# Kernel optimization log

Hardware: AMD Instinct MI355X
Metric: run time of the kernel (lower is better)

The kernel has to match this reference:

```python
import jax, jax.numpy as jnp
import numpy as np
import math

IMG, P, C, D, DEPTH, H, MLP, NCLS, B = 224, 16, 3, 768, 12, 12, 3072, 1000, 32
G = IMG // P          # 14 patches per side
N = G * G             # 196 patches
S = N + 1             # 197 tokens (cls + patches)
DK = D // H
PD = P * P * C        # 768 flattened patch dim


def layer_norm(x, g, b, eps=1e-5):
    mu = jnp.mean(x, axis=-1, keepdims=True)
    var = jnp.mean((x - mu) ** 2, axis=-1, keepdims=True)
    return (x - mu) * jax.lax.rsqrt(var + eps) * g + b


def setup_inputs() -> dict:
    key = jax.random.key(0)
    ks = iter(jax.random.split(key, 32))
    nrm = lambda shape, s=0.02: jax.random.normal(next(ks), shape, jnp.float32) * s
    inp = {
        'x': jax.random.normal(next(ks), (B, C, IMG, IMG), jnp.float32),
        'patch_W': nrm((PD, D)), 'patch_b': jnp.zeros((D,)),
        'cls_token': nrm((1, 1, D)), 'pos_embed': nrm((1, S, D)),
        'Wq': nrm((DEPTH, D, D)), 'bq': jnp.zeros((DEPTH, D)),
        'Wk': nrm((DEPTH, D, D)), 'bk': jnp.zeros((DEPTH, D)),
        'Wv': nrm((DEPTH, D, D)), 'bv': jnp.zeros((DEPTH, D)),
        'Wo': nrm((DEPTH, D, D)), 'bo': jnp.zeros((DEPTH, D)),
        'ln1_g': jnp.ones((DEPTH, D)), 'ln1_b': jnp.zeros((DEPTH, D)),
        'ln2_g': jnp.ones((DEPTH, D)), 'ln2_b': jnp.zeros((DEPTH, D)),
        'W1': nrm((DEPTH, D, MLP)), 'b1': jnp.zeros((DEPTH, MLP)),
        'W2': nrm((DEPTH, MLP, D)), 'b2': jnp.zeros((DEPTH, D)),
        'lnp_g': jnp.ones((D,)), 'lnp_b': jnp.zeros((D,)),
        'head_W': nrm((D, NCLS)), 'head_b': jnp.zeros((NCLS,)),
    }
    return inp


def vit_forward(x, patch_W, patch_b, cls_token, pos_embed,
                Wq, bq, Wk, bk, Wv, bv, Wo, bo,
                ln1_g, ln1_b, ln2_g, ln2_b, W1, b1, W2, b2,
                lnp_g, lnp_b, head_W, head_b):
    b = x.shape[0]
    # faithful replication of torch unfold(2).unfold(3).view: (B,C,G,P,G,P)->(B,C,G,G,P,P)->row-major flatten
    patches = x.reshape(b, C, G, P, G, P).transpose(0, 1, 2, 4, 3, 5).reshape(b, N, PD)
    h = patches @ patch_W + patch_b                              # [B,N,D]
    h = jnp.concatenate([jnp.broadcast_to(cls_token, (b, 1, D)), h], axis=1) + pos_embed
    scale = 1.0 / math.sqrt(DK)
    for i in range(DEPTH):
        y = layer_norm(h, ln1_g[i], ln1_b[i])
        q = (y @ Wq[i] + bq[i]).reshape(b, S, H, DK).transpose(0, 2, 1, 3)
        k = (y @ Wk[i] + bk[i]).reshape(b, S, H, DK).transpose(0, 2, 1, 3)
        v = (y @ Wv[i] + bv[i]).reshape(b, S, H, DK).transpose(0, 2, 1, 3)
        attn = jax.nn.softmax(jnp.einsum('bhqd,bhkd->bhqk', q, k) * scale, axis=-1)
        att = jnp.einsum('bhqk,bhkd->bhqd', attn, v).transpose(0, 2, 1, 3).reshape(b, S, D)
        h = h + att @ Wo[i] + bo[i]
        y = layer_norm(h, ln2_g[i], ln2_b[i])
        h = h + jax.nn.gelu(y @ W1[i] + b1[i], approximate=False) @ W2[i] + b2[i]
    h = layer_norm(h, lnp_g, lnp_b)
    return h[:, 0] @ head_W + head_b                              # [B, NCLS]


def reference(x, patch_W, patch_b, cls_token, pos_embed,
              Wq, bq, Wk, bk, Wv, bv, Wo, bo,
              ln1_g, ln1_b, ln2_g, ln2_b, W1, b1, W2, b2,
              lnp_g, lnp_b, head_W, head_b):
    return vit_forward(x, patch_W, patch_b, cls_token, pos_embed,
                       Wq, bq, Wk, bk, Wv, bv, Wo, bo,
                       ln1_g, ln1_b, ln2_g, ln2_b, W1, b1, W2, b2,
                       lnp_g, lnp_b, head_W, head_b)
```

## Files before the change

kernel.cpp:

```cpp
#include <hip/hip_runtime.h>
#include <hip/hip_bf16.h>


typedef __attribute__((ext_vector_type(8))) short short8;
typedef __attribute__((ext_vector_type(4))) float f32x4;
typedef __attribute__((ext_vector_type(4))) unsigned short us4;

#define MFMA16(a, b, c) __builtin_amdgcn_mfma_f32_16x16x32_bf16(a, b, c, 0, 0, 0)

#define BATCH 32
#define SEQ 197
#define SPAD 208
#define DIM 768
#define HEADS 12
#define DKH 64
#define MLPD 3072
#define NCLS 1000
#define NPATCH 196
#define PDIM 768
#define QKVD 2304
#define ROWS (BATCH * SPAD)
#define WT_ELEMS 7077888

static __device__ __forceinline__ unsigned short f2bf(float f) {
    unsigned int u = __builtin_bit_cast(unsigned int, f);
    u += 0x7fffu + ((u >> 16) & 1u);
    return (unsigned short)(u >> 16);
}

__device__ __forceinline__ void gload16(const void* g, void* l) {
    __builtin_amdgcn_global_load_lds(
        (const __attribute__((address_space(1))) void*)g,
        (__attribute__((address_space(3))) void*)l, 16, 0, 0);
}

__global__ __launch_bounds__(256) void patchify(const float* __restrict__ x,
                                                unsigned short* __restrict__ out) {
    int i = blockIdx.x * 256 + threadIdx.x;
    if (i >= BATCH * NPATCH * PDIM) return;
    int b = i / (NPATCH * PDIM);
    int f = i % (NPATCH * PDIM);
    int c = f / 50176, r = f % 50176;
    int gy = r / 3584, r2 = r % 3584;
    int gx = r2 >> 8, r3 = r2 & 255;
    int py = r3 >> 4, px = r3 & 15;
    float v = x[(((size_t)b * 3 + c) * 224 + gy * 16 + py) * 224 + gx * 16 + px];
    out[i] = f2bf(v);
}

__global__ __launch_bounds__(256) void embed_misc(const float* __restrict__ cls,
                                                  const float* __restrict__ pos,
                                                  float* __restrict__ h) {
    int b = blockIdx.x, t = threadIdx.x;
    float* hb = h + (size_t)b * SPAD * DIM;
    for (int d = t; d < DIM; d += 256) hb[d] = cls[d] + pos[d];
    for (int i = t; i < (SPAD - SEQ) * DIM; i += 256) hb[SEQ * DIM + i] = 0.f;
}

__global__ __launch_bounds__(256) void tconv(const float* __restrict__ src,
                                             unsigned short* __restrict__ dst,
                                             int K, int N) {
    __shared__ float tile[32][33];
    int tn = blockIdx.x, tk = blockIdx.y;
    int t = threadIdx.x, r = t >> 3, c4 = (t & 7) << 2;
    float4 v = *reinterpret_cast<const float4*>(&src[(size_t)(tk * 32 + r) * N + tn * 32 + c4]);
    tile[r][c4 + 0] = v.x; tile[r][c4 + 1] = v.y;
    tile[r][c4 + 2] = v.z; tile[r][c4 + 3] = v.w;
    __syncthreads();
    us4 o = { f2bf(tile[c4 + 0][r]), f2bf(tile[c4 + 1][r]),
              f2bf(tile[c4 + 2][r]), f2bf(tile[c4 + 3][r]) };
    *reinterpret_cast<us4*>(&dst[(size_t)(tn * 32 + r) * K + tk * 32 + c4]) = o;
}

__global__ __launch_bounds__(256) void hconv(const float* __restrict__ src,
                                             unsigned short* __restrict__ dst) {
    __shared__ float tile[32][33];
    int tn = blockIdx.x, tk = blockIdx.y;
    int t = threadIdx.x, r = t >> 3, c4 = (t & 7) << 2;
#pragma unroll
    for (int i = 0; i < 4; ++i) {
        int c = tn * 32 + c4 + i;
        tile[r][c4 + i] = (c < NCLS) ? src[(size_t)(tk * 32 + r) * NCLS + c] : 0.f;
    }
    __syncthreads();
    us4 o = { f2bf(tile[c4 + 0][r]), f2bf(tile[c4 + 1][r]),
              f2bf(tile[c4 + 2][r]), f2bf(tile[c4 + 3][r]) };
    *reinterpret_cast<us4*>(&dst[(size_t)(tn * 32 + r) * 768 + tk * 32 + c4]) = o;
}

__global__ __launch_bounds__(256) void ln_wconv(
    const float* __restrict__ q, const float* __restrict__ k,
    const float* __restrict__ v, const float* __restrict__ o,
    const float* __restrict__ w1, const float* __restrict__ w2,
    unsigned short* __restrict__ wT,
    const float* __restrict__ x, const float* __restrict__ g,
    const float* __restrict__ b, unsigned short* __restrict__ y) {
    if (blockIdx.x < 6912) {
        __shared__ float tile[32][33];
        int tb = blockIdx.x;
        const float* src; unsigned short* dst; int K, N;
        if (tb < 2304) {
            K = 768; N = 768;
            int m = tb / 576; tb -= m * 576;
            src = (m == 0) ? q : (m == 1) ? k : (m == 2) ? v : o;
            dst = wT + (m < 3 ? (size_t)m * 589824 : (size_t)1769472);
        } else if (tb < 4608) {
            tb -= 2304; K = 768; N = 3072; src = w1; dst = wT + 2359296;
        } else {
            tb -= 4608; K = 3072; N = 768; src = w2; dst = wT + 4718592;
        }
        int TN = N >> 5;
        int tn = tb % TN, tk = tb / TN;
        int t = threadIdx.x, r = t >> 3, c4 = (t & 7) << 2;
        float4 vv = *reinterpret_cast<const float4*>(
            &src[(size_t)(tk * 32 + r) * N + tn * 32 + c4]);
        tile[r][c4 + 0] = vv.x; tile[r][c4 + 1] = vv.y;
        tile[r][c4 + 2] = vv.z; tile[r][c4 + 3] = vv.w;
        __syncthreads();
        us4 ov = { f2bf(tile[c4 + 0][r]), f2bf(tile[c4 + 1][r]),
                   f2bf(tile[c4 + 2][r]), f2bf(tile[c4 + 3][r]) };
        *reinterpret_cast<us4*>(&dst[(size_t)(tn * 32 + r) * K + tk * 32 + c4]) = ov;
    } else {
        __shared__ float red[8];
        int row = blockIdx.x - 6912, t = threadIdx.x;
        const float* xr = x + (size_t)row * DIM;
        float v0 = xr[t], v1 = xr[t + 256], v2 = xr[t + 512];
        float s = v0 + v1 + v2, sq = v0 * v0 + v1 * v1 + v2 * v2;
#pragma unroll
        for (int off = 1; off < 64; off <<= 1) {
            s += __shfl_xor(s, off);
            sq += __shfl_xor(sq, off);
        }
        if ((t & 63) == 0) { red[t >> 6] = s; red[4 + (t >> 6)] = sq; }
        __syncthreads();
        s = red[0] + red[1] + red[2] + red[3];
        sq = red[4] + red[5] + red[6] + red[7];
        float mu = s * (1.f / 768.f);
        float var = fmaxf(sq * (1.f / 768.f) - mu * mu, 0.f);
        float rs = rsqrtf(var + 1e-5f);
        unsigned short* yr = y + (size_t)row * DIM;
        yr[t]       = f2bf((v0 - mu) * rs * g[t] + b[t]);
        yr[t + 256] = f2bf((v1 - mu) * rs * g[t + 256] + b[t + 256]);
        yr[t + 512] = f2bf((v2 - mu) * rs * g[t + 512] + b[t + 512]);
    }
}

__global__ __launch_bounds__(256) void pack_bias(const float* __restrict__ bq,
                                                 const float* __restrict__ bk,
                                                 const float* __restrict__ bv,
                                                 float* __restrict__ dst) {
    int i = blockIdx.x * 256 + threadIdx.x;
    if (i >= 12 * QKVD) return;
    int l = i / QKVD, c = i % QKVD;
    float v = (c < 768) ? bq[l * 768 + c]
            : (c < 1536) ? bk[l * 768 + c - 768]
                         : bv[l * 768 + c - 1536];
    dst[i] = v;
}

#define MM1(MF, J, NF) \
    acc[MF][NF] = MFMA16(af[J][0], bfr[NF][0], acc[MF][NF]); \
    acc[MF][NF] = MFMA16(af[J][1], bfr[NF][1], acc[MF][NF]);
#define MMROW(MF, J) MM1(MF, J, 0) MM1(MF, J, 1) MM1(MF, J, 2) MM1(MF, J, 3)

#define WAITVM(N) \
    __builtin_amdgcn_sched_barrier(0); \
    asm volatile("s_waitcnt vmcnt(" #N ")" ::: "memory"); \
    __builtin_amdgcn_sched_barrier(0);

template <int MODE>
__global__ __launch_bounds__(512, 2) void gemm8p(
    const unsigned short* __restrict__ A, const unsigned short* __restrict__ Bt,
    const float* __restrict__ bias, int N, int K,
    unsigned short* __restrict__ outb) {
    __shared__ unsigned short Ab[2][16384];
    __shared__ unsigned short Bb[2][16384];
    const int tid = threadIdx.x, lane = tid & 63, wid = tid >> 6;
    const int wm = wid >> 2, wn = wid & 3;
    const int lr = lane & 15, lg = lane >> 4;
    const int ric = lane >> 3, sswz = (lane & 7) ^ ric;
    const int row0 = blockIdx.x * 256, col0 = blockIdx.y * 256;
    const char* pA = (const char*)A + ((size_t)(row0 + wid * 8 + ric) * K) * 2 + sswz * 16;
    const char* pB = (const char*)Bt + ((size_t)(col0 + wid * 8 + ric) * K) * 2 + sswz * 16;
    const int NT = K >> 6;

    auto stA = [&](int q, int ks, int b) {
        gload16(pA + ((size_t)q * 64 * K + ks) * 2, (char*)&Ab[b][0] + q * 8192 + wid * 1024);
    };
    auto stB = [&](int q, int ks, int b) {
        gload16(pB + ((size_t)q * 64 * K + ks) * 2, (char*)&Bb[b][0] + q * 8192 + wid * 1024);
    };

    f32x4 acc[8][4];
#pragma unroll
    for (int m = 0; m < 8; ++m)
#pragma unroll
        for (int n = 0; n < 4; ++n) acc[m][n] = (f32x4){0.f, 0.f, 0.f, 0.f};

    stB(0, 0, 0); stB(1, 0, 0); stB(2, 0, 0); stB(3, 0, 0);
    stA(0, 0, 0); stA(2, 0, 0); stA(1, 0, 0); stA(3, 0, 0);
    if (NT > 1) {
        stB(0, 64, 1); stB(1, 64, 1); stB(2, 64, 1); stB(3, 64, 1);
        stA(0, 64, 1); stA(2, 64, 1);
        WAITVM(4)
    } else {
        WAITVM(0)
    }
    __builtin_amdgcn_s_barrier();

    const int rsw = lr & 7;
    for (int s = 0; s < NT; ++s) {
        const int d = s & 1;
        const unsigned short* Ad = &Ab[d][0];
        const unsigned short* Bd = &Bb[d][0];
        const bool p1ok = (s + 1 < NT), p2ok = (s + 2 < NT);
        short8 bfr[4][2], af[2][2];
#pragma unroll
        for (int nf = 0; nf < 4; ++nf)
#pragma unroll
            for (int kk = 0; kk < 2; ++kk)
                bfr[nf][kk] = *reinterpret_cast<const short8*>(
                    &Bd[(wn * 64 + nf * 16 + lr) * 64 + (((kk * 4 + lg) ^ rsw) << 3)]);
#pragma unroll
        for (int j = 0; j < 2; ++j)
#pragma unroll
            for (int kk = 0; kk < 2; ++kk)
                af[j][kk] = *reinterpret_cast<const short8*>(
                    &Ad[(wm * 128 + (0 + j) * 16 + lr) * 64 + (((kk * 4 + lg) ^ rsw) << 3)]);
        if (p1ok) { stA(1, (s + 1) * 64, d ^ 1); stA(3, (s + 1) * 64, d ^ 1); }
        __builtin_amdgcn_s_barrier();
        __builtin_amdgcn_s_setprio(1);
        MMROW(0, 0) MMROW(1, 1)
        __builtin_amdgcn_s_setprio(0);
        __builtin_amdgcn_s_barrier();
#pragma unroll
        for (int j = 0; j < 2; ++j)
#pragma unroll
            for (int kk = 0; kk < 2; ++kk)
                af[j][kk] = *reinterpret_cast<const short8*>(
                    &Ad[(wm * 128 + (2 + j) * 16 + lr) * 64 + (((kk * 4 + lg) ^ rsw) << 3)]);
        if (p2ok) { stB(0, (s + 2) * 64, d); stB(1, (s + 2) * 64, d); }
        __builtin_amdgcn_s_barrier();
        __builtin_amdgcn_s_setprio(1);
        MMROW(2, 0) MMROW(3, 1)
        __builtin_amdgcn_s_setprio(0);
        __builtin_amdgcn_s_barrier();
#pragma unroll
        for (int j = 0; j < 2; ++j)
#pragma unroll
            for (int kk = 0; kk < 2; ++kk)
                af[j][kk] = *reinterpret_cast<const short8*>(
                    &Ad[(wm * 128 + (4 + j) * 16 + lr) * 64 + (((kk * 4 + lg) ^ rsw) << 3)]);
        if (p2ok) { stB(2, (s + 2) * 64, d); stB(3, (s + 2) * 64, d); }
        __builtin_amdgcn_s_barrier();
        __builtin_amdgcn_s_setprio(1);
        MMROW(4, 0) MMROW(5, 1)
        __builtin_amdgcn_s_setprio(0);
        __builtin_amdgcn_s_barrier();
#pragma unroll
        for (int j = 0; j < 2; ++j)
#pragma unroll
            for (int kk = 0; kk < 2; ++kk)
                af[j][kk] = *reinterpret_cast<const short8*>(
                    &Ad[(wm * 128 + (6 + j) * 16 + lr) * 64 + (((kk * 4 + lg) ^ rsw) << 3)]);
        if (p2ok) {
            stA(0, (s + 2) * 64, d); stA(2, (s + 2) * 64, d);
            WAITVM(4)
        } else {
            WAITVM(0)
        }
        __builtin_amdgcn_s_barrier();
        __builtin_amdgcn_s_setprio(1);
        MMROW(6, 0) MMROW(7, 1)
        __builtin_amdgcn_s_setprio(0);
        __builtin_amdgcn_s_barrier();
    }
#pragma unroll
    for (int m = 0; m < 8; ++m) {
#pragma unroll
        for (int n = 0; n < 4; ++n) {
            int gcol = col0 + wn * 64 + n * 16 + lr;
            float bv = bias[gcol];
#pragma unroll
            for (int i = 0; i < 4; ++i) {
                int grow = row0 + wm * 128 + m * 16 + lg * 4 + i;
                float v = acc[m][n][i] + bv;
                if (MODE == 2) v = 0.5f * v * (1.f + erff(v * 0.70710678118654752f));
                outb[(size_t)grow * N + gcol] = f2bf(v);
            }
        }
    }
}

template <int BM>
__global__ __launch_bounds__(256) void gemm_tn(
    const unsigned short* __restrict__ A, const unsigned short* __restrict__ Bt,
    const float* __restrict__ bias, int M, int N, int K, int mode,
    unsigned short* __restrict__ outb, float* __restrict__ outf,
    const float* __restrict__ pos) {
    constexpr int MFRAG = BM / 32;
    constexpr int ACH = BM / 8;
    constexpr int TOT = ACH + 16;
    constexpr int CPW = TOT / 4;
    __shared__ unsigned short Alds[BM * 64];
    __shared__ unsigned short Blds[128 * 64];
    const int tid = threadIdx.x, lane = tid & 63, wid = tid >> 6;
    const int row0 = blockIdx.x * BM, col0 = blockIdx.y * 128;
    const int wm = (wid >> 1) * (BM / 2), wn = (wid & 1) * 64;
    const int lr = lane & 15, lg = lane >> 4;
    const int ric = lane >> 3;
    const int sswz = (lane & 7) ^ ric;

    const char* gptr[CPW];
    char* lptr[CPW];
#pragma unroll
    for (int j = 0; j < CPW; ++j) {
        int cc = wid * CPW + j;
        if (cc < ACH) {
            int grow = row0 + cc * 8 + ric;
            gptr[j] = (const char*)A + (size_t)grow * K * 2 + sswz * 16;
            lptr[j] = (char*)Alds + cc * 1024;
        } else {
            int grow = col0 + (cc - ACH) * 8 + ric;
            gptr[j] = (const char*)Bt + (size_t)grow * K * 2 + sswz * 16;
            lptr[j] = (char*)Blds + (cc - ACH) * 1024;
        }
    }

    f32x4 acc[MFRAG][4];
#pragma unroll
    for (int m = 0; m < MFRAG; ++m)
#pragma unroll
        for (int n = 0; n < 4; ++n) acc[m][n] = (f32x4){0.f, 0.f, 0.f, 0.f};

    const int rsw = lr & 7;
    for (int ks = 0; ks < K; ks += 64) {
        __syncthreads();
#pragma unroll
        for (int j = 0; j < CPW; ++j) {
            gload16(gptr[j], lptr[j]);
            gptr[j] += 128;
        }
        __syncthreads();
        short8 af[MFRAG][2], bfr[4][2];
#pragma unroll
        for (int m = 0; m < MFRAG; ++m)
#pragma unroll
            for (int kk = 0; kk < 2; ++kk)
                af[m][kk] = *reinterpret_cast<const short8*>(
                    &Alds[(wm + m * 16 + lr) * 64 + (((kk * 4 + lg) ^ rsw) << 3)]);
#pragma unroll
        for (int n = 0; n < 4; ++n)
#pragma unroll
            for (int kk = 0; kk < 2; ++kk)
                bfr[n][kk] = *reinterpret_cast<const short8*>(
                    &Blds[(wn + n * 16 + lr) * 64 + (((kk * 4 + lg) ^ rsw) << 3)]);
#pragma unroll
        for (int m = 0; m < MFRAG; ++m)
#pragma unroll
            for (int n = 0; n < 4; ++n) {
                acc[m][n] = MFMA16(af[m][0], bfr[n][0], acc[m][n]);
                acc[m][n] = MFMA16(af[m][1], bfr[n][1], acc[m][n]);
            }
    }
#pragma unroll
    for (int m = 0; m < MFRAG; ++m) {
#pragma unroll
        for (int n = 0; n < 4; ++n) {
            int gcol = col0 + wn + n * 16 + lr;
            float bv = bias ? bias[gcol] : 0.f;
#pragma unroll
            for (int i = 0; i < 4; ++i) {
                int grow = row0 + wm + m * 16 + lg * 4 + i;
                float v = acc[m][n][i] + bv;
                if (mode == 0) {
                    outb[(size_t)grow * N + gcol] = f2bf(v);
                } else if (mode == 1) {
                    outf[(size_t)grow * N + gcol] += v;
                } else if (mode == 2) {
                    v = 0.5f * v * (1.f + erff(v * 0.70710678118654752f));
                    outb[(size_t)grow * N + gcol] = f2bf(v);
                } else if (mode == 3) {
                    int pb = grow / NPATCH, pn = grow % NPATCH;
                    size_t o = ((size_t)pb * SPAD + 1 + pn) * DIM + gcol;
                    outf[o] = v + pos[(size_t)(1 + pn) * DIM + gcol];
                } else {
                    if (grow < BATCH && gcol < NCLS)
                        outf[(size_t)grow * NCLS + gcol] = v + pos[gcol];
                }
            }
        }
    }
}

__global__ __launch_bounds__(256) void ln_bf16(const float* __restrict__ x,
                                               const float* __restrict__ g,
                                               const float* __restrict__ b,
                                               unsigned short* __restrict__ y) {
    __shared__ float red[8];
    int row = blockIdx.x, t = threadIdx.x;
    const float* xr = x + (size_t)row * DIM;
    float v0 = xr[t], v1 = xr[t + 256], v2 = xr[t + 512];
    float s = v0 + v1 + v2, sq = v0 * v0 + v1 * v1 + v2 * v2;
#pragma unroll
    for (int off = 1; off < 64; off <<= 1) {
        s += __shfl_xor(s, off);
        sq += __shfl_xor(sq, off);
    }
    if ((t & 63) == 0) { red[t >> 6] = s; red[4 + (t >> 6)] = sq; }
    __syncthreads();
    s = red[0] + red[1] + red[2] + red[3];
    sq = red[4] + red[5] + red[6] + red[7];
    float mu = s * (1.f / 768.f);
    float var = fmaxf(sq * (1.f / 768.f) - mu * mu, 0.f);
    float rs = rsqrtf(var + 1e-5f);
    unsigned short* yr = y + (size_t)row * DIM;
    yr[t]       = f2bf((v0 - mu) * rs * g[t] + b[t]);
    yr[t + 256] = f2bf((v1 - mu) * rs * g[t + 256] + b[t + 256]);
    yr[t + 512] = f2bf((v2 - mu) * rs * g[t + 512] + b[t + 512]);
}

__global__ __launch_bounds__(256) void ln_cls(const float* __restrict__ x,
                                              const float* __restrict__ g,
                                              const float* __restrict__ b,
                                              unsigned short* __restrict__ y) {
    __shared__ float red[8];
    int bb = blockIdx.x, t = threadIdx.x;
    unsigned short* yr = y + (size_t)bb * DIM;
    if (bb >= BATCH) {
        yr[t] = 0; yr[t + 256] = 0; yr[t + 512] = 0;
        return;
    }
    const float* xr = x + (size_t)bb * SPAD * DIM;
    float v0 = xr[t], v1 = xr[t + 256], v2 = xr[t + 512];
    float s = v0 + v1 + v2, sq = v0 * v0 + v1 * v1 + v2 * v2;
#pragma unroll
    for (int off = 1; off < 64; off <<= 1) {
        s += __shfl_xor(s, off);
        sq += __shfl_xor(sq, off);
    }
    if ((t & 63) == 0) { red[t >> 6] = s; red[4 + (t >> 6)] = sq; }
    __syncthreads();
    s = red[0] + red[1] + red[2] + red[3];
    sq = red[4] + red[5] + red[6] + red[7];
    float mu = s * (1.f / 768.f);
    float var = fmaxf(sq * (1.f / 768.f) - mu * mu, 0.f);
    float rs = rsqrtf(var + 1e-5f);
    yr[t]       = f2bf((v0 - mu) * rs * g[t] + b[t]);
    yr[t + 256] = f2bf((v1 - mu) * rs * g[t + 256] + b[t + 256]);
    yr[t + 512] = f2bf((v2 - mu) * rs * g[t + 512] + b[t + 512]);
}

__global__ __launch_bounds__(256) void attn_fused(const unsigned short* __restrict__ qkv,
                                                  unsigned short* __restrict__ att) {
    __shared__ unsigned short Klds[26 * 512];
    __shared__ unsigned short Vlds[64][232];
    __shared__ unsigned short Plds[4][16 * 256];
    int h = blockIdx.x, b = blockIdx.y, tid = threadIdx.x;
    int wid = tid >> 6, lane = tid & 63, lr = lane & 15, lg = lane >> 4;
    const int ric = lane >> 3, sswz = (lane & 7) ^ ric;

    const char* pK = (const char*)qkv +
        ((size_t)(b * SPAD + ric) * QKVD + 768 + h * DKH) * 2 + sswz * 16;
    for (int c = wid; c < 26; c += 4)
        gload16(pK + (size_t)c * 8 * QKVD * 2, (char*)Klds + c * 1024);

    for (int idx = tid; idx < SPAD * 8; idx += 256) {
        int s = idx >> 3, dc = (idx & 7) << 3;
        uint4 w = *reinterpret_cast<const uint4*>(
            &qkv[((size_t)b * SPAD + s) * QKVD + 1536 + h * DKH + dc]);
        const unsigned short* pe = reinterpret_cast<const unsigned short*>(&w);
#pragma unroll
        for (int i = 0; i < 8; ++i) Vlds[dc + i][s] = pe[i];
    }
    for (int i = tid; i < 64 * 24; i += 256) Vlds[i / 24][208 + (i % 24)] = 0;
    __syncthreads();

    unsigned short* Pw = &Plds[wid][0];
    const short8 zero8 = {0, 0, 0, 0, 0, 0, 0, 0};
    const int rowin = lr & 7;

    for (int qt = wid; qt < 13; qt += 4) {
        size_t qoff = ((size_t)b * SPAD + qt * 16 + lr) * QKVD + h * DKH + lg * 8;
        short8 qf0 = *reinterpret_cast<const short8*>(&qkv[qoff]);
        short8 qf1 = *reinterpret_cast<const short8*>(&qkv[qoff + 32]);
        f32x4 acc[13];
#pragma unroll
        for (int kt = 0; kt < 13; ++kt) {
            const unsigned short* kbase = Klds + (kt * 2 + (lr >> 3)) * 512 + rowin * 64;
            short8 kf0 = *reinterpret_cast<const short8*>(&kbase[(lg ^ rowin) << 3]);
            short8 kf1 = *reinterpret_cast<const short8*>(&kbase[((4 + lg) ^ rowin) << 3]);
            f32x4 a = (f32x4){0.f, 0.f, 0.f, 0.f};
            a = MFMA16(qf0, kf0, a);
            a = MFMA16(qf1, kf1, a);
            acc[kt] = a;
        }
#pragma unroll
        for (int kt = 0; kt < 13; ++kt)
#pragma unroll
            for (int r = 0; r < 4; ++r) acc[kt][r] *= 0.125f;
        if (lr >= 5) {
#pragma unroll
            for (int r = 0; r < 4; ++r) acc[12][r] = -1e30f;
        }
        float mx[4] = {-1e30f, -1e30f, -1e30f, -1e30f};
#pragma unroll
        for (int kt = 0; kt < 13; ++kt)
#pragma unroll
            for (int r = 0; r < 4; ++r) mx[r] = fmaxf(mx[r], acc[kt][r]);
#pragma unroll
        for (int r = 0; r < 4; ++r) {
            mx[r] = fmaxf(mx[r], __shfl_xor(mx[r], 1));
            mx[r] = fmaxf(mx[r], __shfl_xor(mx[r], 2));
            mx[r] = fmaxf(mx[r], __shfl_xor(mx[r], 4));
            mx[r] = fmaxf(mx[r], __shfl_xor(mx[r], 8));
        }
        float sm[4] = {0.f, 0.f, 0.f, 0.f};
#pragma unroll
        for (int kt = 0; kt < 13; ++kt)
#pragma unroll
            for (int r = 0; r < 4; ++r) {
                float e = __expf(acc[kt][r] - mx[r]);
                acc[kt][r] = e;
                sm[r] += e;
            }
#pragma unroll
        for (int r = 0; r < 4; ++r) {
            sm[r] += __shfl_xor(sm[r], 1);
            sm[r] += __shfl_xor(sm[r], 2);
            sm[r] += __shfl_xor(sm[r], 4);
            sm[r] += __shfl_xor(sm[r], 8);
        }
#pragma unroll
        for (int r = 0; r < 4; ++r) {
            int row = lg * 4 + r;
            float inv = 1.f / sm[r];
#pragma unroll
            for (int kt = 0; kt < 13; ++kt) {
                int col = kt * 16 + lr;
                int idx = row * 256 + ((((col >> 3) ^ (row & 7)) << 3) | (col & 7));
                Pw[idx] = f2bf(acc[kt][r] * inv);
            }
        }
        if (lr < 6) {
            int s = 26 + lr;
#pragma unroll
            for (int r = 0; r < 4; ++r) {
                int row = lg * 4 + r;
                *reinterpret_cast<short8*>(&Pw[row * 256 + ((s ^ (row & 7)) << 3)]) = zero8;
            }
        }
        int rsw = lr & 7;
#pragma unroll
        for (int dt = 0; dt < 4; ++dt) {
            f32x4 a = (f32x4){0.f, 0.f, 0.f, 0.f};
#pragma unroll
            for (int kk = 0; kk < 7; ++kk) {
                short8 af = *reinterpret_cast<const short8*>(
                    &Pw[lr * 256 + (((kk * 4 + lg) ^ rsw) << 3)]);
                short8 bfr = *reinterpret_cast<const short8*>(
                    &Vlds[dt * 16 + lr][kk * 32 + lg * 8]);
                a = MFMA16(af, bfr, a);
            }
#pragma unroll
            for (int i = 0; i < 4; ++i) {
                int s = qt * 16 + lg * 4 + i;
                att[((size_t)b * SPAD + s) * DIM + h * DKH + dt * 16 + lr] = f2bf(a[i]);
            }
        }
    }
}

extern "C" void kernel_launch(void* const* d_in, const int* in_sizes, int n_in,
                              void* d_out, int out_size, void* d_ws, size_t ws_size,
                              hipStream_t stream) {
    const float* x      = (const float*)d_in[0];
    const float* patchW = (const float*)d_in[1];
    const float* patchB = (const float*)d_in[2];
    const float* clstok = (const float*)d_in[3];
    const float* pose   = (const float*)d_in[4];
    const float* Wq = (const float*)d_in[5];
    const float* bq = (const float*)d_in[6];
    const float* Wk = (const float*)d_in[7];
    const float* bk = (const float*)d_in[8];
    const float* Wv = (const float*)d_in[9];
    const float* bv = (const float*)d_in[10];
    const float* Wo = (const float*)d_in[11];
    const float* bo = (const float*)d_in[12];
    const float* ln1g = (const float*)d_in[13];
    const float* ln1b = (const float*)d_in[14];
    const float* ln2g = (const float*)d_in[15];
    const float* ln2b = (const float*)d_in[16];
    const float* W1 = (const float*)d_in[17];
    const float* b1 = (const float*)d_in[18];
    const float* W2 = (const float*)d_in[19];
    const float* b2 = (const float*)d_in[20];
    const float* lnpg = (const float*)d_in[21];
    const float* lnpb = (const float*)d_in[22];
    const float* headW = (const float*)d_in[23];
    const float* headB = (const float*)d_in[24];
    float* out = (float*)d_out;

    constexpr size_t SZ_H   = (size_t)ROWS * DIM * 4;
    constexpr size_t SZ_QKV = (size_t)ROWS * QKVD * 2;
    constexpr size_t SZ_Y   = (size_t)ROWS * DIM * 2;
    constexpr size_t SZ_M1  = (size_t)ROWS * MLPD * 2;
    constexpr size_t SZ_WT  = (size_t)WT_ELEMS * 2;
    char* w = (char*)d_ws;
    float* hbuf            = (float*)w;
    unsigned short* qkvb   = (unsigned short*)(w + SZ_H);
    unsigned short* ybuf   = (unsigned short*)(w + SZ_H + SZ_QKV);
    unsigned short* m1buf  = (unsigned short*)(w + SZ_H + SZ_QKV + SZ_Y);
    unsigned short* wT     = (unsigned short*)(w + SZ_H + SZ_QKV + SZ_Y + SZ_M1);
    float* bqkv            = (float*)(w + SZ_H + SZ_QKV + SZ_Y + SZ_M1 + SZ_WT);
    unsigned short* patches = m1buf;
    unsigned short* pwT     = ybuf;
    unsigned short* clsbuf  = m1buf;
    unsigned short* hwT     = m1buf + 64 * DIM;

    pack_bias<<<dim3(108), 256, 0, stream>>>(bq, bk, bv, bqkv);

    tconv<<<dim3(24, 24), 256, 0, stream>>>(patchW, pwT, PDIM, DIM);
    patchify<<<dim3((BATCH * NPATCH * PDIM + 255) / 256), 256, 0, stream>>>(x, patches);
    embed_misc<<<dim3(BATCH), 256, 0, stream>>>(clstok, pose, hbuf);
    gemm_tn<64><<<dim3(98, 6), 256, 0, stream>>>(patches, pwT, patchB,
                                                 BATCH * NPATCH, DIM, PDIM, 3,
                                                 nullptr, hbuf, pose);

    for (int i = 0; i < 12; ++i) {
        ln_wconv<<<dim3(6912 + ROWS), 256, 0, stream>>>(
            Wq + (size_t)i * DIM * DIM, Wk + (size_t)i * DIM * DIM,
            Wv + (size_t)i * DIM * DIM, Wo + (size_t)i * DIM * DIM,
            W1 + (size_t)i * DIM * MLPD, W2 + (size_t)i * DIM * MLPD, wT,
            hbuf, ln1g + i * DIM, ln1b + i * DIM, ybuf);
        gemm8p<0><<<dim3(26, 9), 512, 0, stream>>>(ybuf, wT, bqkv + i * QKVD,
                                                   QKVD, DIM, qkvb);
        attn_fused<<<dim3(HEADS, BATCH), 256, 0, stream>>>(qkvb, ybuf);
        gemm_tn<64><<<dim3(104, 6), 256, 0, stream>>>(ybuf, wT + 1769472, bo + i * DIM,
                                                      ROWS, DIM, DIM, 1,
                                                      nullptr, hbuf, nullptr);
        ln_bf16<<<dim3(ROWS), 256, 0, stream>>>(hbuf, ln2g + i * DIM, ln2b + i * DIM, ybuf);
        gemm_tn<128><<<dim3(52, 24), 256, 0, stream>>>(ybuf, wT + 2359296, b1 + i * MLPD,
                                                       ROWS, MLPD, DIM, 2,
                                                       m1buf, nullptr, nullptr);
        gemm_tn<64><<<dim3(104, 6), 256, 0, stream>>>(m1buf, wT + 4718592, b2 + i * DIM,
                                                      ROWS, DIM, MLPD, 1,
                                                      nullptr, hbuf, nullptr);
    }
    ln_cls<<<dim3(64), 256, 0, stream>>>(hbuf, lnpg, lnpb, clsbuf);
    hconv<<<dim3(32, 24), 256, 0, stream>>>(headW, hwT);
    gemm_tn<64><<<dim3(1, 8), 256, 0, stream>>>(clsbuf, hwT, nullptr,
                                                64, 1024, DIM, 4,
                                                nullptr, out, headB);
}
```

Baseline: 2.893 ms.

## Replace 256x256 pipelined QKV GEMM with simpler 128x256 single-buffer kernel

Swaps the QKV projection kernel from a 512-thread, 256x256-tile, double-buffered and prefetched GEMM to a 256-thread kernel with 128x256 tiles and a plain load-sync-compute loop. The grid doubles along M (52x9 blocks), which may fill the CUs better for this small GEMM (K=768, 12 k-steps). It gives up the overlap of global loads with MFMA work and the fine-grained barrier and priority scheduling, so memory latency is now exposed each k-step.

```diff
diff --git a/kernel.cpp b/kernel.cpp
--- a/kernel.cpp
+++ b/kernel.cpp
@@ -158,135 +158,81 @@
     dst[i] = v;
 }
 
-#define MM1(MF, J, NF) \
-    acc[MF][NF] = MFMA16(af[J][0], bfr[NF][0], acc[MF][NF]); \
-    acc[MF][NF] = MFMA16(af[J][1], bfr[NF][1], acc[MF][NF]);
-#define MMROW(MF, J) MM1(MF, J, 0) MM1(MF, J, 1) MM1(MF, J, 2) MM1(MF, J, 3)
-
-#define WAITVM(N) \
-    __builtin_amdgcn_sched_barrier(0); \
-    asm volatile("s_waitcnt vmcnt(" #N ")" ::: "memory"); \
-    __builtin_amdgcn_sched_barrier(0);
-
-template <int MODE>
-__global__ __launch_bounds__(512, 2) void gemm8p(
+__global__ __launch_bounds__(256) void gemm_tn2(
     const unsigned short* __restrict__ A, const unsigned short* __restrict__ Bt,
     const float* __restrict__ bias, int N, int K,
     unsigned short* __restrict__ outb) {
-    __shared__ unsigned short Ab[2][16384];
-    __shared__ unsigned short Bb[2][16384];
+    constexpr int CPW = 12;
+    __shared__ unsigned short Alds[128 * 64];
+    __shared__ unsigned short Blds[256 * 64];
     const int tid = threadIdx.x, lane = tid & 63, wid = tid >> 6;
-    const int wm = wid >> 2, wn = wid & 3;
+    const int row0 = blockIdx.x * 128, col0 = blockIdx.y * 256;
+    const int wm = (wid >> 1) * 64, wn = (wid & 1) * 128;
     const int lr = lane & 15, lg = lane >> 4;
-    const int ric = lane >> 3, sswz = (lane & 7) ^ ric;
-    const int row0 = blockIdx.x * 256, col0 = blockIdx.y * 256;
-    const char* pA = (const char*)A + ((size_t)(row0 + wid * 8 + ric) * K) * 2 + sswz * 16;
-    const char* pB = (const char*)Bt + ((size_t)(col0 + wid * 8 + ric) * K) * 2 + sswz * 16;
-    const int NT = K >> 6;
-
-    auto stA = [&](int q, int ks, int b) {
-        gload16(pA + ((size_t)q * 64 * K + ks) * 2, (char*)&Ab[b][0] + q * 8192 + wid * 1024);
-    };
-    auto stB = [&](int q, int ks, int b) {
-        gload16(pB + ((size_t)q * 64 * K + ks) * 2, (char*)&Bb[b][0] + q * 8192 + wid * 1024);
-    };
-
-    f32x4 acc[8][4];
-#pragma unroll
-    for (int m = 0; m < 8; ++m)
-#pragma unroll
-        for (int n = 0; n < 4; ++n) acc[m][n] = (f32x4){0.f, 0.f, 0.f, 0.f};
-
-    stB(0, 0, 0); stB(1, 0, 0); stB(2, 0, 0); stB(3, 0, 0);
-    stA(0, 0, 0); stA(2, 0, 0); stA(1, 0, 0); stA(3, 0, 0);
-    if (NT > 1) {
-        stB(0, 64, 1); stB(1, 64, 1); stB(2, 64, 1); stB(3, 64, 1);
-        stA(0, 64, 1); stA(2, 64, 1);
-        WAITVM(4)
-    } else {
-        WAITVM(0)
-    }
-    __builtin_amdgcn_s_barrier();
+    const int ric = lane >> 3;
+    const int sswz = (lane & 7) ^ ric;
+
+    const char* gptr[CPW];
+    char* lptr[CPW];
+#pragma unroll
+    for (int j = 0; j < CPW; ++j) {
+        int cc = wid * CPW + j;
+        if (cc < 16) {
+            int grow = row0 + cc * 8 + ric;
+            gptr[j] = (const char*)A + (size_t)grow * K * 2 + sswz * 16;
+            lptr[j] = (char*)Alds + cc * 1024;
+        } else {
+            int grow = col0 + (cc - 16) * 8 + ric;
+            gptr[j] = (const char*)Bt + (size_t)grow * K * 2 + sswz * 16;
+            lptr[j] = (char*)Blds + (cc - 16) * 1024;
+        }
+    }
+
+    f32x4 acc[4][8];
+#pragma unroll
+    for (int m = 0; m < 4; ++m)
+#pragma unroll
+        for (int n = 0; n < 8; ++n) acc[m][n] = (f32x4){0.f, 0.f, 0.f, 0.f};
 
     const int rsw = lr & 7;
-    for (int s = 0; s < NT; ++s) {
-        const int d = s & 1;
-        const unsigned short* Ad = &Ab[d][0];
-        const unsigned short* Bd = &Bb[d][0];
-        const bool p1ok = (s + 1 < NT), p2ok = (s + 2 < NT);
-        short8 bfr[4][2], af[2][2];
-#pragma unroll
-        for (int nf = 0; nf < 4; ++nf)
+    for (int ks = 0; ks < K; ks += 64) {
+        __syncthreads();
+#pragma unroll
+        for (int j = 0; j < CPW; ++j) {
+            gload16(gptr[j], lptr[j]);
+            gptr[j] += 128;
+        }
+        __syncthreads();
+        short8 af[4][2];
+#pragma unroll
+        for (int m = 0; m < 4; ++m)
 #pragma unroll
             for (int kk = 0; kk < 2; ++kk)
-                bfr[nf][kk] = *reinterpret_cast<const short8*>(
-                    &Bd[(wn * 64 + nf * 16 + lr) * 64 + (((kk * 4 + lg) ^ rsw) << 3)]);
-#pragma unroll
-        for (int j = 0; j < 2; ++j)
-#pragma unroll
-            for (int kk = 0; kk < 2; ++kk)
-                af[j][kk] = *reinterpret_cast<const short8*>(
-                    &Ad[(wm * 128 + (0 + j) * 16 + lr) * 64 + (((kk * 4 + lg) ^ rsw) << 3)]);
-        if (p1ok) { stA(1, (s + 1) * 64, d ^ 1); stA(3, (s + 1) * 64, d ^ 1); }
-        __builtin_amdgcn_s_barrier();
-        __builtin_amdgcn_s_setprio(1);
-        MMROW(0, 0) MMROW(1, 1)
-        __builtin_amdgcn_s_setprio(0);
-        __builtin_amdgcn_s_barrier();
-#pragma unroll
-        for (int j = 0; j < 2; ++j)
-#pragma unroll
-            for (int kk = 0; kk < 2; ++kk)
-                af[j][kk] = *reinterpret_cast<const short8*>(
-                    &Ad[(wm * 128 + (2 + j) * 16 + lr) * 64 + (((kk * 4 + lg) ^ rsw) << 3)]);
-        if (p2ok) { stB(0, (s + 2) * 64, d); stB(1, (s + 2) * 64, d); }
-        __builtin_amdgcn_s_barrier();
-        __builtin_amdgcn_s_setprio(1);
-        MMROW(2, 0) MMROW(3, 1)
-        __builtin_amdgcn_s_setprio(0);
-        __builtin_amdgcn_s_barrier();
-#pragma unroll
-        for (int j = 0; j < 2; ++j)
-#pragma unroll
-            for (int kk = 0; kk < 2; ++kk)
-                af[j][kk] = *reinterpret_cast<const short8*>(
-                    &Ad[(wm * 128 + (4 + j) * 16 + lr) * 64 + (((kk * 4 + lg) ^ rsw) << 3)]);
-        if (p2ok) { stB(2, (s + 2) * 64, d); stB(3, (s + 2) * 64, d); }
-        __builtin_amdgcn_s_barrier();
-        __builtin_amdgcn_s_setprio(1);
-        MMROW(4, 0) MMROW(5, 1)
-        __builtin_amdgcn_s_setprio(0);
-        __builtin_amdgcn_s_barrier();
-#pragma unroll
-        for (int j = 0; j < 2; ++j)
-#pragma unroll
-            for (int kk = 0; kk < 2; ++kk)
-                af[j][kk] = *reinterpret_cast<const short8*>(
-                    &Ad[(wm * 128 + (6 + j) * 16 + lr) * 64 + (((kk * 4 + lg) ^ rsw) << 3)]);
-        if (p2ok) {
-            stA(0, (s + 2) * 64, d); stA(2, (s + 2) * 64, d);
-            WAITVM(4)
-        } else {
-            WAITVM(0)
-        }
-        __builtin_amdgcn_s_barrier();
-        __builtin_amdgcn_s_setprio(1);
-        MMROW(6, 0) MMROW(7, 1)
-        __builtin_amdgcn_s_setprio(0);
-        __builtin_amdgcn_s_barrier();
-    }
-#pragma unroll
-    for (int m = 0; m < 8; ++m) {
-#pragma unroll
-        for (int n = 0; n < 4; ++n) {
-            int gcol = col0 + wn * 64 + n * 16 + lr;
+                af[m][kk] = *reinterpret_cast<const short8*>(
+                    &Alds[(wm + m * 16 + lr) * 64 + (((kk * 4 + lg) ^ rsw) << 3)]);
+#pragma unroll
+        for (int n = 0; n < 8; ++n) {
+            short8 b0 = *reinterpret_cast<const short8*>(
+                &Blds[(wn + n * 16 + lr) * 64 + ((lg ^ rsw) << 3)]);
+            short8 b1 = *reinterpret_cast<const short8*>(
+                &Blds[(wn + n * 16 + lr) * 64 + (((4 + lg) ^ rsw) << 3)]);
+#pragma unroll
+            for (int m = 0; m < 4; ++m) {
+                acc[m][n] = MFMA16(af[m][0], b0, acc[m][n]);
+                acc[m][n] = MFMA16(af[m][1], b1, acc[m][n]);
+            }
+        }
+    }
+#pragma unroll
+    for (int m = 0; m < 4; ++m) {
+#pragma unroll
+        for (int n = 0; n < 8; ++n) {
+            int gcol = col0 + wn + n * 16 + lr;
             float bv = bias[gcol];
 #pragma unroll
             for (int i = 0; i < 4; ++i) {
-                int grow = row0 + wm * 128 + m * 16 + lg * 4 + i;
-                float v = acc[m][n][i] + bv;
-                if (MODE == 2) v = 0.5f * v * (1.f + erff(v * 0.70710678118654752f));
-                outb[(size_t)grow * N + gcol] = f2bf(v);
+                int grow = row0 + wm + m * 16 + lg * 4 + i;
+                outb[(size_t)grow * N + gcol] = f2bf(acc[m][n][i] + bv);
             }
         }
     }
@@ -633,8 +579,8 @@
             Wv + (size_t)i * DIM * DIM, Wo + (size_t)i * DIM * DIM,
             W1 + (size_t)i * DIM * MLPD, W2 + (size_t)i * DIM * MLPD, wT,
             hbuf, ln1g + i * DIM, ln1b + i * DIM, ybuf);
-        gemm8p<0><<<dim3(26, 9), 512, 0, stream>>>(ybuf, wT, bqkv + i * QKVD,
-                                                   QKVD, DIM, qkvb);
+        gemm_tn2<<<dim3(52, 9), 256, 0, stream>>>(ybuf, wT, bqkv + i * QKVD,
+                                                  QKVD, DIM, qkvb);
         attn_fused<<<dim3(HEADS, BATCH), 256, 0, stream>>>(qkvb, ybuf);
         gemm_tn<64><<<dim3(104, 6), 256, 0, stream>>>(ybuf, wT + 1769472, bo + i * DIM,
                                                       ROWS, DIM, DIM, 1,
```

New measurement: 3.122 ms. +7.9%, slower.
